# Kernel optimization log

Measured on AMD Instinct MI355X. Metric: run time of the kernel, lower is better.

The kernel has to match this reference:

```python
import jax, jax.numpy as jnp
import numpy as np

B, S, E = 4, 2048, 2048
N_HEADS, HEAD_DIM = 16, 128
NHD = N_HEADS * HEAD_DIM  # n_heads_dim == emb_dim here


def setup_inputs() -> dict:
    key = jax.random.key(0)
    ks = jax.random.split(key, 7)
    s = 0.02
    return {
        "x": jax.random.normal(ks[0], (B, S, E), dtype=jnp.float32),
        # torch nn.Linear weights: [out_features, in_features]
        "w_q": jax.random.normal(ks[1], (NHD, E), dtype=jnp.float32) * s,
        "w_k": jax.random.normal(ks[2], (NHD, E), dtype=jnp.float32) * s,
        "w_v": jax.random.normal(ks[3], (NHD, E), dtype=jnp.float32) * s,
        "w_proj": jax.random.normal(ks[4], (E, NHD), dtype=jnp.float32) * s,
        "b_proj": jax.random.normal(ks[5], (E,), dtype=jnp.float32) * s,
    }


def reference(x, w_q, w_k, w_v, w_proj, b_proj):
    b, s, _ = x.shape
    # projections (torch Linear: y = x @ W^T) -> [b, s, n_heads, head_dim] -> [b, h, s, d]
    def split_heads(y):
        return y.reshape(b, s, N_HEADS, HEAD_DIM).transpose(0, 2, 1, 3)
    q = split_heads(x @ w_q.T)
    k = split_heads(x @ w_k.T)
    v = split_heads(x @ w_v.T)
    scale = 1.0 / np.sqrt(HEAD_DIM).astype(np.float32)
    scores = jnp.einsum("bhsd,bhtd->bhst", q, k) * scale  # [b, h, s, s]
    causal = jnp.tril(jnp.ones((s, s), dtype=bool))
    scores = jnp.where(causal, scores, jnp.finfo(scores.dtype).min)
    attn = jax.nn.softmax(scores, axis=-1)
    out = jnp.einsum("bhst,bhtd->bhsd", attn, v)  # [b, h, s, d]
    out = out.transpose(0, 2, 1, 3).reshape(b, s, NHD)
    return out @ w_proj.T + b_proj
```

## Files before the change

### kernel.cpp

```cpp
#include <hip/hip_runtime.h>

#define LOG2E 1.4426950408889634f
#define ATTN_SCALE 0.08838834764831843f

using bhalf8 = __attribute__((ext_vector_type(8))) short;
using f32x4  = __attribute__((ext_vector_type(4))) float;

__device__ __forceinline__ unsigned short f2bf(float f) {
  unsigned u = __float_as_uint(f);
  u += 0x7fffu + ((u >> 16) & 1u);
  return (unsigned short)(u >> 16);
}

__device__ __forceinline__ unsigned pack_bf16_2(float lo, float hi) {
  unsigned a = __float_as_uint(lo) + 0x8000u;
  unsigned b = __float_as_uint(hi) + 0x8000u;
  return __builtin_amdgcn_perm(b, a, 0x07060302);
}

__device__ __forceinline__ void gl_lds16(const unsigned short* g, unsigned short* l) {
  __builtin_amdgcn_global_load_lds(
      (const __attribute__((address_space(1))) void*)g,
      (__attribute__((address_space(3))) void*)l, 16, 0, 0);
}

__global__ void cvt_kernel(const float* __restrict__ src,
                           unsigned short* __restrict__ dst, int n4) {
  int i = blockIdx.x * blockDim.x + threadIdx.x;
  if (i >= n4) return;
  float4 f = reinterpret_cast<const float4*>(src)[i];
  unsigned lo = (unsigned)f2bf(f.x) | ((unsigned)f2bf(f.y) << 16);
  unsigned hi = (unsigned)f2bf(f.z) | ((unsigned)f2bf(f.w) << 16);
  reinterpret_cast<uint2*>(dst)[i] = make_uint2(lo, hi);
}

#define GBAR()  asm volatile("s_barrier" ::: "memory")
#define GWAITL() do { asm volatile("s_waitcnt lgkmcnt(0)" ::: "memory"); \
                      __builtin_amdgcn_sched_barrier(0); } while (0)

__device__ __forceinline__ bhalf8 ldsfrag(const unsigned short* b, int rb, int kk,
                                          int rbase) {
  return *reinterpret_cast<const bhalf8*>(b + rb * 1024 + kk * 512 + rbase);
}

template <int MODE, int I0, int J0>
__device__ __forceinline__ void mfmaq(f32x4 (&acc)[8][4], const bhalf8 (&afr)[4][2],
                                      const bhalf8 (&bfr)[2][2]) {
#pragma unroll
  for (int kk = 0; kk < 2; ++kk)
#pragma unroll
    for (int i = 0; i < 4; ++i)
#pragma unroll
      for (int j = 0; j < 2; ++j) {
        if (MODE == 1)
          acc[I0 + i][J0 + j] = __builtin_amdgcn_mfma_f32_16x16x32_bf16(
              bfr[j][kk], afr[i][kk], acc[I0 + i][J0 + j], 0, 0, 0);
        else
          acc[I0 + i][J0 + j] = __builtin_amdgcn_mfma_f32_16x16x32_bf16(
              afr[i][kk], bfr[j][kk], acc[I0 + i][J0 + j], 0, 0, 0);
      }
}

__device__ __forceinline__ void stage_half(const unsigned short* __restrict__ M,
                                           unsigned short* dstbase, int h, int ks,
                                           int rowb, int wave, const int (&rdec)[2],
                                           const int (&cdec)[2]) {
#pragma unroll
  for (int ld = 0; ld < 2; ++ld)
    gl_lds16(M + (size_t)(rowb + rdec[ld] + h * 128) * 2048 + ks + cdec[ld],
             dstbase + h * 8192 + ld * 4096 + wave * 512);
}

template <int MODE>
__device__ __forceinline__ void ktile256(
    const unsigned short* __restrict__ A, const unsigned short* __restrict__ Bt,
    unsigned short* as_, unsigned short* bs_, int ks,
    int row0, int col0, int wave, int wr, int wc, int rbase,
    const int (&rdec)[2], const int (&cdec)[2],
    f32x4 (&acc)[8][4], bhalf8 (&af)[4][2], bhalf8 (&bfA)[2][2], bhalf8 (&bfB)[2][2]) {
#pragma unroll
  for (int i = 0; i < 4; ++i)
#pragma unroll
    for (int kk = 0; kk < 2; ++kk) af[i][kk] = ldsfrag(as_, wr * 8 + i, kk, rbase);
#pragma unroll
  for (int j = 0; j < 2; ++j)
#pragma unroll
    for (int kk = 0; kk < 2; ++kk) bfA[j][kk] = ldsfrag(bs_, wc * 4 + j, kk, rbase);
  GBAR(); GWAITL();
  __builtin_amdgcn_s_setprio(1);
  mfmaq<MODE, 0, 0>(acc, af, bfA);
  __builtin_amdgcn_s_setprio(0);
  GBAR();
#pragma unroll
  for (int j = 0; j < 2; ++j)
#pragma unroll
    for (int kk = 0; kk < 2; ++kk) bfB[j][kk] = ldsfrag(bs_, wc * 4 + 2 + j, kk, rbase);
  GBAR(); GWAITL();
  __builtin_amdgcn_s_setprio(1);
  mfmaq<MODE, 0, 2>(acc, af, bfB);
  __builtin_amdgcn_s_setprio(0);
  GBAR();
#pragma unroll
  for (int i = 0; i < 4; ++i)
#pragma unroll
    for (int kk = 0; kk < 2; ++kk) af[i][kk] = ldsfrag(as_, wr * 8 + 4 + i, kk, rbase);
  stage_half(Bt, bs_, 0, ks, col0, wave, rdec, cdec);
  stage_half(Bt, bs_, 1, ks, col0, wave, rdec, cdec);
  GBAR(); GWAITL();
  __builtin_amdgcn_s_setprio(1);
  mfmaq<MODE, 4, 2>(acc, af, bfB);
  __builtin_amdgcn_s_setprio(0);
  GBAR();
  stage_half(A,  as_, 0, ks, row0, wave, rdec, cdec);
  stage_half(A,  as_, 1, ks, row0, wave, rdec, cdec);
  GBAR();
  __builtin_amdgcn_s_setprio(1);
  mfmaq<MODE, 4, 0>(acc, af, bfA);
  __builtin_amdgcn_s_setprio(0);
  asm volatile("s_waitcnt vmcnt(8)" ::: "memory");
  GBAR();
}

template <int MODE>
__global__ __launch_bounds__(512, 2) void gemm256_bt(
    const unsigned short* __restrict__ A,
    const unsigned short* __restrict__ Bt,
    unsigned short* __restrict__ obf, float* __restrict__ of32,
    const float* __restrict__ bias) {
  __shared__ __align__(16) unsigned short As[2][16384];
  __shared__ __align__(16) unsigned short Bs[2][16384];
  const int tid  = threadIdx.x;
  const int lane = tid & 63;
  const int wave = tid >> 6;
  const int quad = lane >> 4;
  const int c16  = lane & 15;
  const int wr = wave >> 2, wc = wave & 3;

  const int wg  = blockIdx.y * 8 + blockIdx.x;
  const int xcd = wg & 7;
  const int idx = wg >> 3;
  const int row0 = (xcd * 4 + (idx >> 3)) * 256;
  const int col0 = (idx & 7) * 256;

  const int rbase = c16 * 32 + ((quad * 8) ^ ((c16 >> 3) << 4));

  int rdec[2], cdec[2];
#pragma unroll
  for (int ld = 0; ld < 2; ++ld) {
    const int c = ld * 512 + tid;
    rdec[ld] = ((c >> 7) << 4) + ((c >> 2) & 15);
    cdec[ld] = (((c >> 6) & 1) << 5) + (((c & 3) << 3) ^ (((c >> 5) & 1) << 4));
  }

  f32x4 acc[8][4];
#pragma unroll
  for (int i = 0; i < 8; ++i)
#pragma unroll
    for (int j = 0; j < 4; ++j)
#pragma unroll
      for (int r = 0; r < 4; ++r) acc[i][j][r] = 0.0f;

  bhalf8 af[4][2], bfA[2][2], bfB[2][2];

  stage_half(Bt, Bs[0], 0, 0,  col0, wave, rdec, cdec);
  stage_half(Bt, Bs[0], 1, 0,  col0, wave, rdec, cdec);
  stage_half(A,  As[0], 0, 0,  row0, wave, rdec, cdec);
  stage_half(A,  As[0], 1, 0,  row0, wave, rdec, cdec);
  stage_half(Bt, Bs[1], 0, 64, col0, wave, rdec, cdec);
  stage_half(Bt, Bs[1], 1, 64, col0, wave, rdec, cdec);
  stage_half(A,  As[1], 0, 64, row0, wave, rdec, cdec);
  stage_half(A,  As[1], 1, 64, row0, wave, rdec, cdec);
  asm volatile("s_waitcnt vmcnt(8)" ::: "memory");
  GBAR();

#pragma unroll 1
  for (int it = 0; it < 16; ++it) {
    const int kA  = it * 128;
    const int ksA = (kA + 128 > 1984) ? 1984 : kA + 128;
    const int ksB = (kA + 192 > 1984) ? 1984 : kA + 192;
    ktile256<MODE>(A, Bt, As[0], Bs[0], ksA, row0, col0, wave, wr, wc, rbase,
                   rdec, cdec, acc, af, bfA, bfB);
    ktile256<MODE>(A, Bt, As[1], Bs[1], ksB, row0, col0, wave, wr, wc, rbase,
                   rdec, cdec, acc, af, bfA, bfB);
  }

#pragma unroll
  for (int i = 0; i < 8; ++i)
#pragma unroll
    for (int j = 0; j < 4; ++j)
#pragma unroll
      for (int r = 0; r < 4; ++r) {
        float v = acc[i][j][r];
        if (MODE == 2) {
          int m = row0 + wr * 128 + i * 16 + quad * 4 + r;
          int n = col0 + wc * 64 + j * 16 + c16;
          of32[(size_t)m * 2048 + n] = v + bias[n];
        } else if (MODE == 0) {
          int m = row0 + wr * 128 + i * 16 + quad * 4 + r;
          int n = col0 + wc * 64 + j * 16 + c16;
          int b = m >> 11, s = m & 2047;
          int h = n >> 7,  d = n & 127;
          obf[(((size_t)(b * 16 + h)) * 2048 + s) * 128 + d] = f2bf(v);
        } else {
          int n = col0 + wc * 64 + j * 16 + quad * 4 + r;
          int m = row0 + wr * 128 + i * 16 + c16;
          int b = m >> 11, s = m & 2047;
          int h = n >> 7,  d = n & 127;
          obf[(((size_t)(b * 16 + h)) * 128 + d) * 2048 + s] = f2bf(v);
        }
      }
}

#define LQK 136
#define LV   72
__global__ __launch_bounds__(256, 4) void flash_kernel(
    const unsigned short* __restrict__ Q,
    const unsigned short* __restrict__ K,
    const unsigned short* __restrict__ Vt,
    unsigned short* __restrict__ O) {
  const int tid  = threadIdx.x;
  const int lane = tid & 63;
  const int wave = tid >> 6;
  const int quad = lane >> 4;
  const int c16  = lane & 15;
  const int bh = blockIdx.x;
  const int q0 = (31 - blockIdx.y) * 64;
  const int bb = bh >> 4, hh = bh & 15;
  const int qidx = q0 + wave * 16 + c16;
  const float SL = ATTN_SCALE * LOG2E;

  __shared__ __align__(16) unsigned short Ks[64 * LQK];
  __shared__ __align__(16) unsigned short Vs[128 * LV];

  const unsigned short* Qg = Q + ((size_t)bh * 2048 + q0) * 128;
#pragma unroll
  for (int i = 0; i < 4; i++) {
    int chunk = i * 256 + tid;
    int t = chunk >> 4, dc = (chunk & 15) << 3;
    *reinterpret_cast<bhalf8*>(Ks + t * LQK + dc) =
        *reinterpret_cast<const bhalf8*>(Qg + chunk * 8);
  }
  __syncthreads();
  bhalf8 qb[4];
#pragma unroll
  for (int kk = 0; kk < 4; kk++)
    qb[kk] = *reinterpret_cast<const bhalf8*>(Ks + (wave * 16 + c16) * LQK + kk * 32 + quad * 8);

  f32x4 o_acc[8];
#pragma unroll
  for (int jd = 0; jd < 8; jd++)
#pragma unroll
    for (int r = 0; r < 4; r++) o_acc[jd][r] = 0.0f;
  float m_i = -__builtin_inff(), l_i = 0.0f;

  const unsigned short* Kbh = K  + (size_t)bh * 2048 * 128;
  const unsigned short* Vbh = Vt + (size_t)bh * 128 * 2048;

  const int nt = q0 / 64 + 1;
  for (int it = 0; it < nt; ++it) {
    const int t0 = it * 64;
    bhalf8 rk[4], rv[4];
#pragma unroll
    for (int i = 0; i < 4; i++) {
      int chunk = i * 256 + tid;
      int t = chunk >> 4, dc = (chunk & 15) << 3;
      rk[i] = *reinterpret_cast<const bhalf8*>(Kbh + (size_t)(t0 + t) * 128 + dc);
      int d = chunk >> 3, tc = (chunk & 7) << 3;
      rv[i] = *reinterpret_cast<const bhalf8*>(Vbh + (size_t)d * 2048 + t0 + tc);
    }
    __syncthreads();
#pragma unroll
    for (int i = 0; i < 4; i++) {
      int chunk = i * 256 + tid;
      int t = chunk >> 4, dc = (chunk & 15) << 3;
      int row = (((t >> 5) << 1) | ((t >> 2) & 1)) * 16 + ((t >> 3) & 3) * 4 + (t & 3);
      *reinterpret_cast<bhalf8*>(Ks + row * LQK + dc) = rk[i];
      int d = chunk >> 3, tc = (chunk & 7) << 3;
      *reinterpret_cast<bhalf8*>(Vs + d * LV + tc) = rv[i];
    }
    __syncthreads();

    f32x4 st[4];
#pragma unroll
    for (int tt = 0; tt < 4; tt++)
#pragma unroll
      for (int r = 0; r < 4; r++) st[tt][r] = 0.0f;
#pragma unroll
    for (int kk = 0; kk < 4; kk++)
#pragma unroll
      for (int tt = 0; tt < 4; tt++) {
        bhalf8 ka = *reinterpret_cast<const bhalf8*>(Ks + (tt * 16 + c16) * LQK + kk * 32 + quad * 8);
        st[tt] = __builtin_amdgcn_mfma_f32_16x16x32_bf16(ka, qb[kk], st[tt], 0, 0, 0);
      }

    const bool diag = (t0 == q0);
    float pv[4][4];
    float rmax = -__builtin_inff();
#pragma unroll
    for (int tt = 0; tt < 4; tt++)
#pragma unroll
      for (int r = 0; r < 4; r++) {
        float x = st[tt][r];
        if (diag) {
          int t = t0 + ((tt >> 1) << 5) + (quad << 3) + ((tt & 1) << 2) + r;
          if (t > qidx) x = -__builtin_inff();
        }
        pv[tt][r] = x;
        rmax = fmaxf(rmax, x);
      }
    rmax = fmaxf(rmax, __shfl_xor(rmax, 16));
    rmax = fmaxf(rmax, __shfl_xor(rmax, 32));
    const float pmax_s = rmax * SL;

    if (__any(pmax_s > m_i + 8.0f)) {
      const float mnew = fmaxf(m_i, pmax_s);
      const float alpha = exp2f(m_i - mnew);
      m_i = mnew;
      l_i *= alpha;
#pragma unroll
      for (int jd = 0; jd < 8; jd++)
#pragma unroll
        for (int r = 0; r < 4; r++) o_acc[jd][r] *= alpha;
    }

    float rs = 0.0f;
#pragma unroll
    for (int tt = 0; tt < 4; tt++)
#pragma unroll
      for (int r = 0; r < 4; r++) {
        float p = exp2f(__builtin_fmaf(pv[tt][r], SL, -m_i));
        pv[tt][r] = p;
        rs += p;
      }
    l_i += rs;

#pragma unroll
    for (int u = 0; u < 2; u++) {
      union { bhalf8 h; uint4 w; } pu;
      pu.w.x = pack_bf16_2(pv[2 * u][0],     pv[2 * u][1]);
      pu.w.y = pack_bf16_2(pv[2 * u][2],     pv[2 * u][3]);
      pu.w.z = pack_bf16_2(pv[2 * u + 1][0], pv[2 * u + 1][1]);
      pu.w.w = pack_bf16_2(pv[2 * u + 1][2], pv[2 * u + 1][3]);
#pragma unroll
      for (int jd = 0; jd < 8; jd++) {
        bhalf8 va = *reinterpret_cast<const bhalf8*>(Vs + (jd * 16 + c16) * LV + u * 32 + quad * 8);
        o_acc[jd] = __builtin_amdgcn_mfma_f32_16x16x32_bf16(va, pu.h, o_acc[jd], 0, 0, 0);
      }
    }
  }

  l_i += __shfl_xor(l_i, 16);
  l_i += __shfl_xor(l_i, 32);
  const float inv = 1.0f / l_i;
#pragma unroll
  for (int jd = 0; jd < 8; jd++) {
    unsigned lo = (unsigned)f2bf(o_acc[jd][0] * inv) | ((unsigned)f2bf(o_acc[jd][1] * inv) << 16);
    unsigned hi = (unsigned)f2bf(o_acc[jd][2] * inv) | ((unsigned)f2bf(o_acc[jd][3] * inv) << 16);
    *reinterpret_cast<uint2*>(O + ((size_t)(bb * 2048 + qidx)) * 2048 + hh * 128 + jd * 16 + quad * 4) =
        make_uint2(lo, hi);
  }
}

extern "C" void kernel_launch(void* const* d_in, const int* in_sizes, int n_in,
                              void* d_out, int out_size, void* d_ws, size_t ws_size,
                              hipStream_t stream) {
  const float* x  = (const float*)d_in[0];
  const float* wq = (const float*)d_in[1];
  const float* wk = (const float*)d_in[2];
  const float* wv = (const float*)d_in[3];
  const float* wp = (const float*)d_in[4];
  const float* bp = (const float*)d_in[5];
  float* out = (float*)d_out;

  unsigned short* ws  = (unsigned short*)d_ws;
  const size_t ME = (size_t)8192 * 2048;
  const size_t EE = (size_t)2048 * 2048;
  unsigned short* xb  = ws;
  unsigned short* wqb = xb  + ME;
  unsigned short* wkb = wqb + EE;
  unsigned short* wvb = wkb + EE;
  unsigned short* wpb = wvb + EE;
  unsigned short* Qb  = wpb + EE;
  unsigned short* Kb  = Qb  + ME;
  unsigned short* Vtb = Kb  + ME;
  unsigned short* Ob  = Vtb + ME;

  cvt_kernel<<<16384, 256, 0, stream>>>(x,  xb,  (int)(ME / 4));
  cvt_kernel<<<4096,  256, 0, stream>>>(wq, wqb, (int)(EE / 4));
  cvt_kernel<<<4096,  256, 0, stream>>>(wk, wkb, (int)(EE / 4));
  cvt_kernel<<<4096,  256, 0, stream>>>(wv, wvb, (int)(EE / 4));
  cvt_kernel<<<4096,  256, 0, stream>>>(wp, wpb, (int)(EE / 4));

  dim3 g2(8, 32);
  gemm256_bt<0><<<g2, 512, 0, stream>>>(xb, wqb, Qb,  nullptr, nullptr);
  gemm256_bt<0><<<g2, 512, 0, stream>>>(xb, wkb, Kb,  nullptr, nullptr);
  gemm256_bt<1><<<g2, 512, 0, stream>>>(xb, wvb, Vtb, nullptr, nullptr);

  flash_kernel<<<dim3(64, 32), 256, 0, stream>>>(Qb, Kb, Vtb, Ob);

  gemm256_bt<2><<<g2, 512, 0, stream>>>(Ob, wpb, nullptr, out, bp);
}
```

Measured before the change: 565.1 us.

## Prefetch next K/V tile into registers during flash attention compute

Restructures the flash-attention loop so global loads for the next K/V tile are issued into a second register set right after the current tile is stored to LDS. The loop is unrolled by two and alternates register buffers, so load latency overlaps with the QK and PV MFMA work. It also raises wave priority around the MFMA blocks with s_setprio. The extra prefetch registers raise VGPR pressure and may hurt occupancy at the 4-blocks launch bound.

```diff
diff --git a/kernel.cpp b/kernel.cpp
--- a/kernel.cpp
+++ b/kernel.cpp
@@ -213,6 +213,115 @@
 
 #define LQK 136
 #define LV   72
+__device__ __forceinline__ void fl_load(const unsigned short* __restrict__ Kbh,
+                                        const unsigned short* __restrict__ Vbh,
+                                        int t0, int tid,
+                                        bhalf8 (&rk)[4], bhalf8 (&rv)[4]) {
+#pragma unroll
+  for (int i = 0; i < 4; i++) {
+    int chunk = i * 256 + tid;
+    int t = chunk >> 4, dc = (chunk & 15) << 3;
+    rk[i] = *reinterpret_cast<const bhalf8*>(Kbh + (size_t)(t0 + t) * 128 + dc);
+    int d = chunk >> 3, tc = (chunk & 7) << 3;
+    rv[i] = *reinterpret_cast<const bhalf8*>(Vbh + (size_t)d * 2048 + t0 + tc);
+  }
+}
+
+__device__ __forceinline__ void fl_tile(
+    const unsigned short* __restrict__ Kbh, const unsigned short* __restrict__ Vbh,
+    unsigned short* Ks, unsigned short* Vs,
+    const bhalf8 (&qb)[4], f32x4 (&o_acc)[8], float& m_i, float& l_i,
+    bhalf8 (&rk)[4], bhalf8 (&rv)[4], bhalf8 (&nk)[4], bhalf8 (&nv)[4],
+    int it, int nt, int q0, int tid, int quad, int c16, int qidx) {
+  const int t0 = it * 64;
+  const float SL = ATTN_SCALE * LOG2E;
+  __syncthreads();
+#pragma unroll
+  for (int i = 0; i < 4; i++) {
+    int chunk = i * 256 + tid;
+    int t = chunk >> 4, dc = (chunk & 15) << 3;
+    int row = (((t >> 5) << 1) | ((t >> 2) & 1)) * 16 + ((t >> 3) & 3) * 4 + (t & 3);
+    *reinterpret_cast<bhalf8*>(Ks + row * LQK + dc) = rk[i];
+    int d = chunk >> 3, tc = (chunk & 7) << 3;
+    *reinterpret_cast<bhalf8*>(Vs + d * LV + tc) = rv[i];
+  }
+  __syncthreads();
+
+  if (it + 1 < nt) fl_load(Kbh, Vbh, t0 + 64, tid, nk, nv);
+
+  f32x4 st[4];
+#pragma unroll
+  for (int tt = 0; tt < 4; tt++)
+#pragma unroll
+    for (int r = 0; r < 4; r++) st[tt][r] = 0.0f;
+  __builtin_amdgcn_s_setprio(1);
+#pragma unroll
+  for (int kk = 0; kk < 4; kk++)
+#pragma unroll
+    for (int tt = 0; tt < 4; tt++) {
+      bhalf8 ka = *reinterpret_cast<const bhalf8*>(Ks + (tt * 16 + c16) * LQK + kk * 32 + quad * 8);
+      st[tt] = __builtin_amdgcn_mfma_f32_16x16x32_bf16(ka, qb[kk], st[tt], 0, 0, 0);
+    }
+  __builtin_amdgcn_s_setprio(0);
+
+  const bool diag = (t0 == q0);
+  float pv[4][4];
+  float rmax = -__builtin_inff();
+#pragma unroll
+  for (int tt = 0; tt < 4; tt++)
+#pragma unroll
+    for (int r = 0; r < 4; r++) {
+      float x = st[tt][r];
+      if (diag) {
+        int t = t0 + ((tt >> 1) << 5) + (quad << 3) + ((tt & 1) << 2) + r;
+        if (t > qidx) x = -__builtin_inff();
+      }
+      pv[tt][r] = x;
+      rmax = fmaxf(rmax, x);
+    }
+  rmax = fmaxf(rmax, __shfl_xor(rmax, 16));
+  rmax = fmaxf(rmax, __shfl_xor(rmax, 32));
+  const float pmax_s = rmax * SL;
+
+  if (__any(pmax_s > m_i + 8.0f)) {
+    const float mnew = fmaxf(m_i, pmax_s);
+    const float alpha = exp2f(m_i - mnew);
+    m_i = mnew;
+    l_i *= alpha;
+#pragma unroll
+    for (int jd = 0; jd < 8; jd++)
+#pragma unroll
+      for (int r = 0; r < 4; r++) o_acc[jd][r] *= alpha;
+  }
+
+  float rs = 0.0f;
+#pragma unroll
+  for (int tt = 0; tt < 4; tt++)
+#pragma unroll
+    for (int r = 0; r < 4; r++) {
+      float p = exp2f(__builtin_fmaf(pv[tt][r], SL, -m_i));
+      pv[tt][r] = p;
+      rs += p;
+    }
+  l_i += rs;
+
+#pragma unroll
+  for (int u = 0; u < 2; u++) {
+    union { bhalf8 h; uint4 w; } pu;
+    pu.w.x = pack_bf16_2(pv[2 * u][0],     pv[2 * u][1]);
+    pu.w.y = pack_bf16_2(pv[2 * u][2],     pv[2 * u][3]);
+    pu.w.z = pack_bf16_2(pv[2 * u + 1][0], pv[2 * u + 1][1]);
+    pu.w.w = pack_bf16_2(pv[2 * u + 1][2], pv[2 * u + 1][3]);
+    __builtin_amdgcn_s_setprio(1);
+#pragma unroll
+    for (int jd = 0; jd < 8; jd++) {
+      bhalf8 va = *reinterpret_cast<const bhalf8*>(Vs + (jd * 16 + c16) * LV + u * 32 + quad * 8);
+      o_acc[jd] = __builtin_amdgcn_mfma_f32_16x16x32_bf16(va, pu.h, o_acc[jd], 0, 0, 0);
+    }
+    __builtin_amdgcn_s_setprio(0);
+  }
+}
+
 __global__ __launch_bounds__(256, 4) void flash_kernel(
     const unsigned short* __restrict__ Q,
     const unsigned short* __restrict__ K,
@@ -227,10 +336,16 @@
   const int q0 = (31 - blockIdx.y) * 64;
   const int bb = bh >> 4, hh = bh & 15;
   const int qidx = q0 + wave * 16 + c16;
-  const float SL = ATTN_SCALE * LOG2E;
 
   __shared__ __align__(16) unsigned short Ks[64 * LQK];
   __shared__ __align__(16) unsigned short Vs[128 * LV];
+
+  const unsigned short* Kbh = K  + (size_t)bh * 2048 * 128;
+  const unsigned short* Vbh = Vt + (size_t)bh * 128 * 2048;
+  const int nt = q0 / 64 + 1;
+
+  bhalf8 rkA[4], rvA[4], rkB[4], rvB[4];
+  fl_load(Kbh, Vbh, 0, tid, rkA, rvA);
 
   const unsigned short* Qg = Q + ((size_t)bh * 2048 + q0) * 128;
 #pragma unroll
@@ -253,100 +368,15 @@
     for (int r = 0; r < 4; r++) o_acc[jd][r] = 0.0f;
   float m_i = -__builtin_inff(), l_i = 0.0f;
 
-  const unsigned short* Kbh = K  + (size_t)bh * 2048 * 128;
-  const unsigned short* Vbh = Vt + (size_t)bh * 128 * 2048;
-
-  const int nt = q0 / 64 + 1;
-  for (int it = 0; it < nt; ++it) {
-    const int t0 = it * 64;
-    bhalf8 rk[4], rv[4];
-#pragma unroll
-    for (int i = 0; i < 4; i++) {
-      int chunk = i * 256 + tid;
-      int t = chunk >> 4, dc = (chunk & 15) << 3;
-      rk[i] = *reinterpret_cast<const bhalf8*>(Kbh + (size_t)(t0 + t) * 128 + dc);
-      int d = chunk >> 3, tc = (chunk & 7) << 3;
-      rv[i] = *reinterpret_cast<const bhalf8*>(Vbh + (size_t)d * 2048 + t0 + tc);
-    }
-    __syncthreads();
-#pragma unroll
-    for (int i = 0; i < 4; i++) {
-      int chunk = i * 256 + tid;
-      int t = chunk >> 4, dc = (chunk & 15) << 3;
-      int row = (((t >> 5) << 1) | ((t >> 2) & 1)) * 16 + ((t >> 3) & 3) * 4 + (t & 3);
-      *reinterpret_cast<bhalf8*>(Ks + row * LQK + dc) = rk[i];
-      int d = chunk >> 3, tc = (chunk & 7) << 3;
-      *reinterpret_cast<bhalf8*>(Vs + d * LV + tc) = rv[i];
-    }
-    __syncthreads();
-
-    f32x4 st[4];
-#pragma unroll
-    for (int tt = 0; tt < 4; tt++)
-#pragma unroll
-      for (int r = 0; r < 4; r++) st[tt][r] = 0.0f;
-#pragma unroll
-    for (int kk = 0; kk < 4; kk++)
-#pragma unroll
-      for (int tt = 0; tt < 4; tt++) {
-        bhalf8 ka = *reinterpret_cast<const bhalf8*>(Ks + (tt * 16 + c16) * LQK + kk * 32 + quad * 8);
-        st[tt] = __builtin_amdgcn_mfma_f32_16x16x32_bf16(ka, qb[kk], st[tt], 0, 0, 0);
-      }
-
-    const bool diag = (t0 == q0);
-    float pv[4][4];
-    float rmax = -__builtin_inff();
-#pragma unroll
-    for (int tt = 0; tt < 4; tt++)
-#pragma unroll
-      for (int r = 0; r < 4; r++) {
-        float x = st[tt][r];
-        if (diag) {
-          int t = t0 + ((tt >> 1) << 5) + (quad << 3) + ((tt & 1) << 2) + r;
-          if (t > qidx) x = -__builtin_inff();
-        }
-        pv[tt][r] = x;
-        rmax = fmaxf(rmax, x);
-      }
-    rmax = fmaxf(rmax, __shfl_xor(rmax, 16));
-    rmax = fmaxf(rmax, __shfl_xor(rmax, 32));
-    const float pmax_s = rmax * SL;
-
-    if (__any(pmax_s > m_i + 8.0f)) {
-      const float mnew = fmaxf(m_i, pmax_s);
-      const float alpha = exp2f(m_i - mnew);
-      m_i = mnew;
-      l_i *= alpha;
-#pragma unroll
-      for (int jd = 0; jd < 8; jd++)
-#pragma unroll
-        for (int r = 0; r < 4; r++) o_acc[jd][r] *= alpha;
-    }
-
-    float rs = 0.0f;
-#pragma unroll
-    for (int tt = 0; tt < 4; tt++)
-#pragma unroll
-      for (int r = 0; r < 4; r++) {
-        float p = exp2f(__builtin_fmaf(pv[tt][r], SL, -m_i));
-        pv[tt][r] = p;
-        rs += p;
-      }
-    l_i += rs;
-
-#pragma unroll
-    for (int u = 0; u < 2; u++) {
-      union { bhalf8 h; uint4 w; } pu;
-      pu.w.x = pack_bf16_2(pv[2 * u][0],     pv[2 * u][1]);
-      pu.w.y = pack_bf16_2(pv[2 * u][2],     pv[2 * u][3]);
-      pu.w.z = pack_bf16_2(pv[2 * u + 1][0], pv[2 * u + 1][1]);
-      pu.w.w = pack_bf16_2(pv[2 * u + 1][2], pv[2 * u + 1][3]);
-#pragma unroll
-      for (int jd = 0; jd < 8; jd++) {
-        bhalf8 va = *reinterpret_cast<const bhalf8*>(Vs + (jd * 16 + c16) * LV + u * 32 + quad * 8);
-        o_acc[jd] = __builtin_amdgcn_mfma_f32_16x16x32_bf16(va, pu.h, o_acc[jd], 0, 0, 0);
-      }
-    }
+  int it = 0;
+#pragma unroll 1
+  for (;;) {
+    fl_tile(Kbh, Vbh, Ks, Vs, qb, o_acc, m_i, l_i,
+            rkA, rvA, rkB, rvB, it, nt, q0, tid, quad, c16, qidx);
+    if (++it == nt) break;
+    fl_tile(Kbh, Vbh, Ks, Vs, qb, o_acc, m_i, l_i,
+            rkB, rvB, rkA, rvA, it, nt, q0, tid, quad, c16, qidx);
+    if (++it == nt) break;
   }
 
   l_i += __shfl_xor(l_i, 16);
```

Measured after the change: 976.2 us. 72.7% more time.
